# Optimization experiments

Measured on AMD Instinct MI355X. Metric: run time of the kernel, lower is better.

## Reference

```python
import jax, jax.numpy as jnp
import numpy as np

K = 2  # DGL TAGConv default number of hops
N_GRAPHS = 64


def _tag_conv(h, src, dst, W, b, norm):
    # TAGConv: concat [h, A_hat h, A_hat^2 h] @ W + b, A_hat = D^-1/2 A D^-1/2
    n = h.shape[0]
    hops = [h]
    cur = h
    for _ in range(K):
        msg = (cur * norm)[src]                      # gather from src, [E, d]
        agg = jnp.zeros_like(cur).at[dst].add(msg)   # scatter-sum to dst
        cur = agg * norm
        hops.append(cur)
    z = jnp.concatenate(hops, axis=-1)               # [N, (K+1)*d]
    return jax.nn.relu(z @ W + b)


def _norm(dst, n):
    deg = jnp.zeros((n,), jnp.float32).at[dst].add(1.0)
    deg = jnp.clip(deg, 1.0, None)
    return (deg ** -0.5)[:, None]                    # [N, 1]


def setup_inputs() -> dict:
    key = jax.random.key(0)
    ks = jax.random.split(key, 8)
    N, E, IN, HID, C = 100000, 3200000, 128, 256, 10
    h = jax.random.normal(ks[0], (N, IN), jnp.float32)
    src = jax.random.randint(ks[1], (E,), 0, N, jnp.int32)
    dst = jax.random.randint(ks[2], (E,), 0, N, jnp.int32)
    graph_ids = jnp.sort(jax.random.randint(ks[3], (N,), 0, N_GRAPHS, jnp.int32))
    s1 = ((K + 1) * IN) ** -0.5
    s2 = ((K + 1) * HID) ** -0.5
    W1 = jax.random.normal(ks[4], ((K + 1) * IN, HID), jnp.float32) * s1
    b1 = jnp.zeros((HID,), jnp.float32)
    W2 = jax.random.normal(ks[5], ((K + 1) * HID, HID), jnp.float32) * s2
    b2 = jnp.zeros((HID,), jnp.float32)
    Wc = jax.random.normal(ks[6], (HID, C), jnp.float32) * (HID ** -0.5)
    bc = jnp.zeros((C,), jnp.float32)
    return {"h": h, "src": src, "dst": dst, "graph_ids": graph_ids,
            "W1": W1, "b1": b1, "W2": W2, "b2": b2, "Wc": Wc, "bc": bc}


def reference(h, src, dst, graph_ids, W1, b1, W2, b2, Wc, bc):
    n = h.shape[0]
    norm = _norm(dst, n)
    x = _tag_conv(h, src, dst, W1, b1, norm)
    x = _tag_conv(x, src, dst, W2, b2, norm)
    pooled = jax.ops.segment_max(x, graph_ids, num_segments=N_GRAPHS)  # [G, HID]
    return pooled @ Wc + bc                                            # [G, C]
```

## Files before the change

kernel.cpp:

```cpp
#include <hip/hip_runtime.h>
#include <hip/hip_bf16.h>


typedef unsigned short u16;
typedef unsigned int u32;
typedef unsigned char u8;

__device__ inline float u2f(u16 u) { return __uint_as_float(((u32)u) << 16); }
__device__ inline u16 f2u(float f) {
    __hip_bfloat16 b = __float2bfloat16(f);
    return *reinterpret_cast<u16*>(&b);
}


constexpr int NPB = 128, NC = 128, NBMAX = 784;

__global__ __launch_bounds__(256) void countA_kernel(
    const int* __restrict__ dst, int* __restrict__ Hmat, int E, int CS, int NB) {
    __shared__ int hist[NBMAX];
    int tid = threadIdx.x;
    for (int b = tid; b < NB; b += 256) hist[b] = 0;
    __syncthreads();
    int base = blockIdx.x * CS;
    int end = base + CS < E ? base + CS : E;
    for (int i = base + tid; i < end; i += 256) {
        int d = __builtin_nontemporal_load(dst + i);
        atomicAdd(&hist[d >> 7], 1);
    }
    __syncthreads();
    for (int b = tid; b < NB; b += 256) Hmat[b * NC + blockIdx.x] = hist[b];
}

__global__ __launch_bounds__(256) void scatterC_kernel(
    const int* __restrict__ src, const int* __restrict__ dst,
    const int* __restrict__ Omat, uint2* __restrict__ Earr,
    int E, int CS, int NB) {
    __shared__ int cur[NBMAX];
    int tid = threadIdx.x;
    int c = blockIdx.x;
    for (int b = tid; b < NB; b += 256) cur[b] = Omat[b * NC + c];
    __syncthreads();
    int base = c * CS;
    int end = base + CS < E ? base + CS : E;
    for (int i = base + tid; i < end; i += 256) {
        int d = __builtin_nontemporal_load(dst + i);
        int s = __builtin_nontemporal_load(src + i);
        int pos = atomicAdd(&cur[d >> 7], 1);
        uint2 e;
        e.x = (u32)s;
        e.y = (u32)(d & (NPB - 1));
        Earr[pos] = e;
    }
}

__global__ __launch_bounds__(256) void fineD_kernel(
    const uint2* __restrict__ Earr, const int* __restrict__ Omat,
    int* __restrict__ colidx, int* __restrict__ rowptr,
    float* __restrict__ normv, int N, int E, int NB) {
    __shared__ int cnt[NPB];
    __shared__ int scn[NPB];
    __shared__ int cur2[NPB];
    int tid = threadIdx.x;
    int b = blockIdx.x;
    int base = Omat[b * NC];
    int end = Omat[(b + 1) * NC];
    if (tid < NPB) cnt[tid] = 0;
    __syncthreads();
    for (int i = base + tid; i < end; i += 256)
        atomicAdd(&cnt[Earr[i].y], 1);
    __syncthreads();
    if (tid < NPB) scn[tid] = cnt[tid];
    __syncthreads();
    for (int off = 1; off < NPB; off <<= 1) {
        int v = (tid < NPB && tid >= off) ? scn[tid - off] : 0;
        __syncthreads();
        if (tid < NPB) scn[tid] += v;
        __syncthreads();
    }
    int node0 = b * NPB;
    if (tid < NPB) {
        int excl = scn[tid] - cnt[tid];
        cur2[tid] = base + excl;
        int node = node0 + tid;
        if (node < N) {
            rowptr[node] = base + excl;
            int d = cnt[tid];
            float fd = d < 1 ? 1.0f : (float)d;
            normv[node] = rsqrtf(fd);
        }
    }
    if (b == 0 && tid == 0) rowptr[N] = E;
    __syncthreads();
    for (int i = base + tid; i < end; i += 256) {
        uint2 e = Earr[i];
        int pos = atomicAdd(&cur2[e.y], 1);
        colidx[pos] = (int)e.x;
    }
}

__global__ void scan1_kernel(const int* __restrict__ in, int* __restrict__ outp,
                             int* __restrict__ bsum, int n) {
    __shared__ int sd[1024];
    int t = threadIdx.x;
    int i = blockIdx.x * 1024 + t;
    int v = (i < n) ? in[i] : 0;
    sd[t] = v;
    __syncthreads();
    for (int off = 1; off < 1024; off <<= 1) {
        int x = (t >= off) ? sd[t - off] : 0;
        __syncthreads();
        sd[t] += x;
        __syncthreads();
    }
    if (i < n) outp[i] = sd[t] - v;
    if (t == 1023) bsum[blockIdx.x] = sd[t];
}

__global__ void scan2_kernel(int* __restrict__ bsum, int nb) {
    __shared__ int sd[1024];
    int t = threadIdx.x;
    int v = (t < nb) ? bsum[t] : 0;
    sd[t] = v;
    __syncthreads();
    for (int off = 1; off < 1024; off <<= 1) {
        int x = (t >= off) ? sd[t - off] : 0;
        __syncthreads();
        sd[t] += x;
        __syncthreads();
    }
    if (t < nb) bsum[t] = sd[t] - v;
}

__global__ void scan3_kernel(int* __restrict__ outp, const int* __restrict__ bsum,
                             int n, int E) {
    int i = blockIdx.x * blockDim.x + threadIdx.x;
    if (i < n) outp[i] += bsum[i >> 10];
    if (i == 0) outp[n] = E;
}


struct alignas(4) U2 { u16 v[2]; };
struct alignas(8) U4 { u16 v[4]; };
struct alignas(16) U8 { u16 v[8]; };


__global__ __launch_bounds__(256) void castquant_f32_128(
    const float* __restrict__ h, u16* __restrict__ cat, int ldcat,
    const float* __restrict__ normv,
    u8* __restrict__ q, float* __restrict__ m, int N) {
    int row = blockIdx.x * 4 + (threadIdx.x >> 6);
    if (row >= N) return;
    int lane = threadIdx.x & 63;
    float2 f = *(const float2*)(h + (size_t)row * 128 + lane * 2);
    U2 o;
    o.v[0] = f2u(f.x);
    o.v[1] = f2u(f.y);
    *(U2*)(cat + (size_t)row * ldcat + lane * 2) = o;
    float mx = fmaxf(fabsf(f.x), fabsf(f.y));
    #pragma unroll
    for (int off = 32; off > 0; off >>= 1)
        mx = fmaxf(mx, __shfl_xor(mx, off, 64));
    float inv = mx > 0.f ? 127.f / mx : 0.f;
    u32 q0 = (u32)((int)rintf(f.x * inv) + 128);
    u32 q1 = (u32)((int)rintf(f.y * inv) + 128);
    *(unsigned short*)(q + (size_t)row * 128 + lane * 2) =
        (unsigned short)(q0 | (q1 << 8));
    if (lane == 0) m[row] = normv[row] * (mx * (1.f / 127.f));
}


__global__ __launch_bounds__(256) void quant_bf16_256(
    const u16* __restrict__ x, const float* __restrict__ normv,
    u8* __restrict__ q, float* __restrict__ m, int N) {
    int row = blockIdx.x * 4 + (threadIdx.x >> 6);
    if (row >= N) return;
    int lane = threadIdx.x & 63;
    U4 v = *(const U4*)(x + (size_t)row * 256 + lane * 4);
    float f[4];
    #pragma unroll
    for (int i = 0; i < 4; ++i) f[i] = u2f(v.v[i]);
    float mx = fmaxf(fmaxf(fabsf(f[0]), fabsf(f[1])),
                     fmaxf(fabsf(f[2]), fabsf(f[3])));
    #pragma unroll
    for (int off = 32; off > 0; off >>= 1)
        mx = fmaxf(mx, __shfl_xor(mx, off, 64));
    float inv = mx > 0.f ? 127.f / mx : 0.f;
    u32 b0 = (u32)((int)rintf(f[0] * inv) + 128);
    u32 b1 = (u32)((int)rintf(f[1] * inv) + 128);
    u32 b2 = (u32)((int)rintf(f[2] * inv) + 128);
    u32 b3 = (u32)((int)rintf(f[3] * inv) + 128);
    *(u32*)(q + (size_t)row * 256 + lane * 4) =
        b0 | (b1 << 8) | (b2 << 16) | (b3 << 24);
    if (lane == 0) m[row] = normv[row] * (mx * (1.f / 127.f));
}


template <int BPL, int QOUT>
__global__ __launch_bounds__(256, 2) void prop_q8_kernel(
    const u8* __restrict__ qin, const float* __restrict__ m,
    u16* __restrict__ out, int ldout,
    const int* __restrict__ rowptr, const int* __restrict__ colidx,
    const float* __restrict__ normv, int N,
    u8* __restrict__ qout, float* __restrict__ mout) {
    constexpr int D = 32 * BPL;
    constexpr int NW = BPL / 4;
    constexpr int UE = 8;
    int node = blockIdx.x * 4 + (threadIdx.x >> 6);
    if (node >= N) return;
    const int lane = threadIdx.x & 63;
    const int half = lane >> 5;
    const int l32 = lane & 31;
    const u32 laneoff = (u32)l32 * BPL;
    int s = rowptr[node], e = rowptr[node + 1];
    float acc[BPL];
    #pragma unroll
    for (int q = 0; q < BPL; ++q) acc[q] = 0.f;
    float msum = 0.f;
    const int nfull = (e - s) >> 4;
    int p = s;
    if (nfull > 0) {
        int c[UE];
        #pragma unroll
        for (int u = 0; u < UE; ++u) c[u] = colidx[s + 2 * u + half];
        for (int g = 0; g < nfull; ++g) {
            u32 w[UE][NW];
            #pragma unroll
            for (int u = 0; u < UE; ++u) {
                u32 off = (u32)c[u] * D + laneoff;
                if (BPL == 8) {
                    uint2 gg = *(const uint2*)(qin + off);
                    w[u][0] = gg.x; w[u][1] = gg.y;
                } else {
                    w[u][0] = *(const u32*)(qin + off);
                }
            }
            float nm[UE];
            #pragma unroll
            for (int u = 0; u < UE; ++u) nm[u] = m[c[u]];
            if (g + 1 < nfull) {
                int pn = s + (g + 1) * 16;
                #pragma unroll
                for (int u = 0; u < UE; ++u) c[u] = colidx[pn + 2 * u + half];
            }
            #pragma unroll
            for (int u = 0; u < UE; ++u) {
                msum += nm[u];
                #pragma unroll
                for (int t = 0; t < NW; ++t) {
                    u32 ww = w[u][t];
                    acc[4 * t + 0] += nm[u] * (float)(ww & 0xffu);
                    acc[4 * t + 1] += nm[u] * (float)((ww >> 8) & 0xffu);
                    acc[4 * t + 2] += nm[u] * (float)((ww >> 16) & 0xffu);
                    acc[4 * t + 3] += nm[u] * (float)(ww >> 24);
                }
            }
        }
        p = s + nfull * 16;
    }
    if (p < e) {
        const int el = e - 1;
        int c[UE];
        #pragma unroll
        for (int u = 0; u < UE; ++u) {
            int idx = p + 2 * u + half;
            c[u] = colidx[idx < e ? idx : el];
        }
        u32 w[UE][NW];
        #pragma unroll
        for (int u = 0; u < UE; ++u) {
            u32 off = (u32)c[u] * D + laneoff;
            if (BPL == 8) {
                uint2 gg = *(const uint2*)(qin + off);
                w[u][0] = gg.x; w[u][1] = gg.y;
            } else {
                w[u][0] = *(const u32*)(qin + off);
            }
        }
        float nm[UE];
        #pragma unroll
        for (int u = 0; u < UE; ++u) {
            int idx = p + 2 * u + half;
            float mm = m[c[u]];
            nm[u] = idx < e ? mm : 0.f;
        }
        #pragma unroll
        for (int u = 0; u < UE; ++u) {
            msum += nm[u];
            #pragma unroll
            for (int t = 0; t < NW; ++t) {
                u32 ww = w[u][t];
                acc[4 * t + 0] += nm[u] * (float)(ww & 0xffu);
                acc[4 * t + 1] += nm[u] * (float)((ww >> 8) & 0xffu);
                acc[4 * t + 2] += nm[u] * (float)((ww >> 16) & 0xffu);
                acc[4 * t + 3] += nm[u] * (float)(ww >> 24);
            }
        }
    }
    #pragma unroll
    for (int q = 0; q < BPL; ++q) acc[q] += __shfl_xor(acc[q], 32, 64);
    msum += __shfl_xor(msum, 32, 64);
    float nn = normv[node];
    #pragma unroll
    for (int q = 0; q < BPL; ++q) acc[q] = nn * (acc[q] - 128.f * msum);
    if (half == 0) {
        if (BPL == 8) {
            U8 o;
            #pragma unroll
            for (int q = 0; q < 8; ++q) o.v[q] = f2u(acc[q]);
            *(U8*)(out + (size_t)node * ldout + l32 * 8) = o;
        } else {
            U4 o;
            #pragma unroll
            for (int q = 0; q < 4; ++q) o.v[q] = f2u(acc[q]);
            *(U4*)(out + (size_t)node * ldout + l32 * 4) = o;
        }
    }
    if (QOUT) {
        float mx = 0.f;
        #pragma unroll
        for (int q = 0; q < BPL; ++q) mx = fmaxf(mx, fabsf(acc[q]));
        #pragma unroll
        for (int off = 16; off > 0; off >>= 1)
            mx = fmaxf(mx, __shfl_xor(mx, off, 64));
        float inv = mx > 0.f ? 127.f / mx : 0.f;
        if (half == 0) {
            u32 b[BPL > 4 ? 8 : 4];
            #pragma unroll
            for (int q = 0; q < BPL; ++q)
                b[q] = (u32)((int)rintf(acc[q] * inv) + 128);
            if (BPL == 8) {
                uint2 g;
                g.x = b[0] | (b[1] << 8) | (b[2] << 16) | (b[3] << 24);
                g.y = b[4] | (b[5] << 8) | (b[6] << 16) | (b[7] << 24);
                *(uint2*)(qout + (size_t)node * D + l32 * 8) = g;
            } else {
                *(u32*)(qout + (size_t)node * D + l32 * 4) =
                    b[0] | (b[1] << 8) | (b[2] << 16) | (b[3] << 24);
            }
            if (lane == 0) mout[node] = nn * (mx * (1.f / 127.f));
        }
    }
}


typedef __attribute__((ext_vector_type(8))) short bf16x8f;
typedef __attribute__((ext_vector_type(4))) float f32x4;

__device__ inline void async16(const void* g, void* l) {
    __builtin_amdgcn_global_load_lds(
        (__attribute__((address_space(1))) void*)(g),
        (__attribute__((address_space(3))) void*)(l), 16, 0, 0);
}

constexpr int GBM = 128, GBN = 64, GBK = 32;

__device__ inline void stageA_sw(const u16* __restrict__ A, int lda, int row0,
                                 int k0, u16* dst, int tid) {
    #pragma unroll
    for (int i = 0; i < 2; ++i) {
        int c = tid + i * 256;
        int row = c >> 2;
        int seg = (c & 3) ^ ((row >> 1) & 3);
        async16(A + (size_t)(row0 + row) * lda + k0 + seg * 8, dst + c * 8);
    }
}

template <int KK>
__global__ __launch_bounds__(256) void gemm_mfma(
    const u16* __restrict__ A, int lda,
    const u16* __restrict__ Bt,
    const u16* __restrict__ Cadd,
    const float* __restrict__ bias,
    u16* __restrict__ Cout,
    int M, int relu) {
    constexpr int KC = KK / 8;
    __shared__ u16 Ab[2][GBM * GBK];
    __shared__ u16 Bs[GBN * KK];
    const int tid = threadIdx.x;
    const int lane = tid & 63;
    const int wave = tid >> 6;
    const int wm = wave >> 1, wn = wave & 1;
    const int row0 = blockIdx.x * GBM;
    const int col0 = blockIdx.y * GBN;
    const int NOUT = 256;

    {
        const u16* srcB = Bt + (size_t)col0 * KK;
        #pragma unroll
        for (int i = 0; i < GBN * KC / 256; ++i) {
            int cb = tid + i * 256;
            int n = cb / KC;
            int j = (cb % KC) ^ (n & 7);
            async16(srcB + (size_t)n * KK + j * 8, &Bs[cb * 8]);
        }
    }
    stageA_sw(A, lda, row0, 0, Ab[0], tid);
    __syncthreads();

    f32x4 acc[4][2];
    #pragma unroll
    for (int mi = 0; mi < 4; ++mi)
        #pragma unroll
        for (int ni = 0; ni < 2; ++ni) acc[mi][ni] = (f32x4)0.f;

    constexpr int nk = KK / GBK;
    const int mb = lane & 15;
    const int seg = lane >> 4;
    for (int ks = 0; ks < nk; ++ks) {
        int cur = ks & 1;
        if (ks + 1 < nk) stageA_sw(A, lda, row0, (ks + 1) * GBK, Ab[cur ^ 1], tid);
        bf16x8f a[4], b[2];
        #pragma unroll
        for (int mi = 0; mi < 4; ++mi) {
            int r = wm * 64 + mi * 16 + mb;
            int ca = r * 4 + (seg ^ ((r >> 1) & 3));
            a[mi] = *(const bf16x8f*)&Ab[cur][ca * 8];
        }
        #pragma unroll
        for (int ni = 0; ni < 2; ++ni) {
            int n = wn * 32 + ni * 16 + mb;
            int jk = ks * 4 + seg;
            int cb = n * KC + (jk ^ (n & 7));
            b[ni] = *(const bf16x8f*)&Bs[cb * 8];
        }
        #pragma unroll
        for (int mi = 0; mi < 4; ++mi)
            #pragma unroll
            for (int ni = 0; ni < 2; ++ni)
                acc[mi][ni] = __builtin_amdgcn_mfma_f32_16x16x32_bf16(
                    a[mi], b[ni], acc[mi][ni], 0, 0, 0);
        __syncthreads();
    }

    #pragma unroll
    for (int mi = 0; mi < 4; ++mi) {
        #pragma unroll
        for (int r = 0; r < 4; ++r) {
            int row = row0 + wm * 64 + mi * 16 + (lane >> 4) * 4 + r;
            if (row < M) {
                #pragma unroll
                for (int ni = 0; ni < 2; ++ni) {
                    int col = col0 + wn * 32 + ni * 16 + (lane & 15);
                    float v = acc[mi][ni][r];
                    if (Cadd) v += u2f(Cadd[(size_t)row * NOUT + col]);
                    if (bias) v += bias[col];
                    if (relu) v = fmaxf(v, 0.f);
                    Cout[(size_t)row * NOUT + col] = f2u(v);
                }
            }
        }
    }
}

__global__ void transpose_cast(const float* __restrict__ W, u16* __restrict__ Wt,
                               int K, int Nn) {
    int idx = blockIdx.x * blockDim.x + threadIdx.x;
    if (idx < K * Nn) {
        int n = idx / K, k = idx % K;
        Wt[idx] = f2u(W[(size_t)k * Nn + n]);
    }
}


__global__ void pool_kernel(const u16* __restrict__ x, const int* __restrict__ gid,
                            float* __restrict__ pooled, int N, int HID) {
    int t = threadIdx.x;
    int n0 = blockIdx.x * 128;
    int n1 = n0 + 128 < N ? n0 + 128 : N;
    float cur = 0.f;
    int cg = gid[n0];
    for (int n = n0; n < n1; ++n) {
        int g = gid[n];
        if (g != cg) {
            atomicMax((int*)&pooled[(size_t)cg * HID + t], __float_as_int(cur));
            cg = g;
            cur = 0.f;
        }
        float v = u2f(x[(size_t)n * HID + t]);
        cur = cur > v ? cur : v;
    }
    atomicMax((int*)&pooled[(size_t)cg * HID + t], __float_as_int(cur));
}

__global__ void head_kernel(const float* __restrict__ pooled, const float* __restrict__ Wc,
                            const float* __restrict__ bc, float* __restrict__ out,
                            int HID, int C) {
    __shared__ float row[256];
    int g = blockIdx.x;
    int t = threadIdx.x;
    if (t < HID) row[t] = pooled[(size_t)g * HID + t];
    __syncthreads();
    if (t < C) {
        float s = bc[t];
        for (int k = 0; k < HID; ++k) s += row[k] * Wc[(size_t)k * C + t];
        out[(size_t)g * C + t] = s;
    }
}


extern "C" void kernel_launch(void* const* d_in, const int* in_sizes, int n_in,
                              void* d_out, int out_size, void* d_ws, size_t ws_size,
                              hipStream_t stream) {
    const float* h  = (const float*)d_in[0];
    const int* src  = (const int*)d_in[1];
    const int* dst  = (const int*)d_in[2];
    const int* gid  = (const int*)d_in[3];
    const float* W1 = (const float*)d_in[4];
    const float* b1 = (const float*)d_in[5];
    const float* W2 = (const float*)d_in[6];
    const float* b2 = (const float*)d_in[7];
    const float* Wc = (const float*)d_in[8];
    const float* bc = (const float*)d_in[9];
    float* out = (float*)d_out;

    const int N   = in_sizes[3];
    const int E   = in_sizes[1];
    const int IN  = in_sizes[0] / N;
    const int HID = in_sizes[5];
    const int C   = in_sizes[9];
    const int G   = out_size / C;
    const int CAT = 3 * IN;
    const int Mpad = (N + 127) & ~127;
    const int NB = (N + NPB - 1) / NPB;
    const int CS = (E + NC - 1) / NC;

    char* wp = (char*)d_ws;
    auto alloc = [&](size_t bytes) {
        char* p = wp;
        wp += (bytes + 255) & ~(size_t)255;
        return p;
    };
    float* pooled = (float*)alloc((size_t)G * HID * sizeof(float));
    float* normv  = (float*)alloc((size_t)N * sizeof(float));
    float* mv     = (float*)alloc((size_t)N * sizeof(float));
    float* mv2    = (float*)alloc((size_t)N * sizeof(float));
    int* rowptr   = (int*)alloc((size_t)(N + 1) * sizeof(int));
    int* bsum     = (int*)alloc(1024 * sizeof(int));
    int* Omat     = (int*)alloc((size_t)(NB * NC + 1) * sizeof(int));
    int* Hmat     = (int*)alloc((size_t)(NB * NC) * sizeof(int));
    int* colidx   = (int*)alloc((size_t)E * sizeof(int));
    u16* Wt1      = (u16*)alloc((size_t)CAT * HID * sizeof(u16));
    u16* Wt2      = (u16*)alloc((size_t)3 * HID * HID * sizeof(u16));
    u16* CAT1     = (u16*)alloc((size_t)Mpad * CAT * sizeof(u16));
    u16* X1       = (u16*)alloc((size_t)Mpad * HID * sizeof(u16));
    u16* B2       = (u16*)alloc((size_t)Mpad * HID * sizeof(u16));
    u16* B1       = CAT1;
    uint2* Earr   = (uint2*)CAT1;
    u8* Q8L2      = (u8*)(CAT1 + (size_t)Mpad * HID);
    u8* Q8A       = (u8*)B2;
    u8* Q8B       = (u8*)B2 + (size_t)Mpad * 128;

    const int n2 = NB * NC;
    countA_kernel<<<NC, 256, 0, stream>>>(dst, Hmat, E, CS, NB);
    scan1_kernel<<<(n2 + 1023) / 1024, 1024, 0, stream>>>(Hmat, Omat, bsum, n2);
    scan2_kernel<<<1, 1024, 0, stream>>>(bsum, (n2 + 1023) / 1024);
    scan3_kernel<<<(n2 + 255) / 256, 256, 0, stream>>>(Omat, bsum, n2, E);
    scatterC_kernel<<<NC, 256, 0, stream>>>(src, dst, Omat, Earr, E, CS, NB);
    fineD_kernel<<<NB, 256, 0, stream>>>(Earr, Omat, colidx, rowptr, normv, N, E, NB);

    transpose_cast<<<(CAT * HID + 255) / 256, 256, 0, stream>>>(W1, Wt1, CAT, HID);
    for (int s2 = 0; s2 < 3; ++s2)
        transpose_cast<<<(HID * HID + 255) / 256, 256, 0, stream>>>(
            W2 + (size_t)s2 * HID * HID, Wt2 + (size_t)s2 * HID * HID, HID, HID);

    int pb = (N + 3) / 4;
    castquant_f32_128<<<pb, 256, 0, stream>>>(h, CAT1, CAT, normv, Q8A, mv, N);
    prop_q8_kernel<4, 1><<<pb, 256, 0, stream>>>(Q8A, mv, CAT1 + IN, CAT,
                                                 rowptr, colidx, normv, N, Q8B, mv2);
    prop_q8_kernel<4, 0><<<pb, 256, 0, stream>>>(Q8B, mv2, CAT1 + 2 * IN, CAT,
                                                 rowptr, colidx, normv, N,
                                                 nullptr, nullptr);
    dim3 ggrid(Mpad / GBM, HID / GBN);
    gemm_mfma<384><<<ggrid, 256, 0, stream>>>(CAT1, CAT, Wt1, nullptr, b1, X1, N, 1);

    gemm_mfma<256><<<ggrid, 256, 0, stream>>>(X1, HID, Wt2 + (size_t)2 * HID * HID,
                                              nullptr, nullptr, B1, N, 0);
    quant_bf16_256<<<pb, 256, 0, stream>>>(B1, normv, Q8L2, mv, N);
    prop_q8_kernel<8, 0><<<pb, 256, 0, stream>>>(Q8L2, mv, B2, HID,
                                                 rowptr, colidx, normv, N,
                                                 nullptr, nullptr);
    gemm_mfma<256><<<ggrid, 256, 0, stream>>>(X1, HID, Wt2 + (size_t)HID * HID,
                                              B2, nullptr, B1, N, 0);
    quant_bf16_256<<<pb, 256, 0, stream>>>(B1, normv, Q8L2, mv, N);
    prop_q8_kernel<8, 0><<<pb, 256, 0, stream>>>(Q8L2, mv, B2, HID,
                                                 rowptr, colidx, normv, N,
                                                 nullptr, nullptr);
    gemm_mfma<256><<<ggrid, 256, 0, stream>>>(X1, HID, Wt2, B2, b2, B1, N, 1);

    hipMemsetAsync(pooled, 0, (size_t)G * HID * sizeof(float), stream);
    pool_kernel<<<(N + 127) / 128, HID, 0, stream>>>(B1, gid, pooled, N, HID);
    head_kernel<<<G, HID, 0, stream>>>(pooled, Wc, bc, out, HID, C);
}
```

Before: 1.045 ms.

## Fuse int8 quantization into GEMM epilogue with per-32-column scales, remap grid

Removes the separate quant_bf16_256 pass by quantizing GEMM outputs to int8 directly in the epilogue. Scales are now computed per 32-column group, so each row has 8 scale factors, and the propagation kernel reads the scale for its lane's column group. The GEMM is also launched as a 1D grid with an XCD-aware block remapping. This avoids writing and re-reading the bf16 intermediate, at the cost of extra shuffles, an LDS staging pass in the epilogue, and 8x more scale reads in propagation.

```diff
diff --git a/kernel.cpp b/kernel.cpp
--- a/kernel.cpp
+++ b/kernel.cpp
@@ -169,33 +169,7 @@
 }
 
 
-__global__ __launch_bounds__(256) void quant_bf16_256(
-    const u16* __restrict__ x, const float* __restrict__ normv,
-    u8* __restrict__ q, float* __restrict__ m, int N) {
-    int row = blockIdx.x * 4 + (threadIdx.x >> 6);
-    if (row >= N) return;
-    int lane = threadIdx.x & 63;
-    U4 v = *(const U4*)(x + (size_t)row * 256 + lane * 4);
-    float f[4];
-    #pragma unroll
-    for (int i = 0; i < 4; ++i) f[i] = u2f(v.v[i]);
-    float mx = fmaxf(fmaxf(fabsf(f[0]), fabsf(f[1])),
-                     fmaxf(fabsf(f[2]), fabsf(f[3])));
-    #pragma unroll
-    for (int off = 32; off > 0; off >>= 1)
-        mx = fmaxf(mx, __shfl_xor(mx, off, 64));
-    float inv = mx > 0.f ? 127.f / mx : 0.f;
-    u32 b0 = (u32)((int)rintf(f[0] * inv) + 128);
-    u32 b1 = (u32)((int)rintf(f[1] * inv) + 128);
-    u32 b2 = (u32)((int)rintf(f[2] * inv) + 128);
-    u32 b3 = (u32)((int)rintf(f[3] * inv) + 128);
-    *(u32*)(q + (size_t)row * 256 + lane * 4) =
-        b0 | (b1 << 8) | (b2 << 16) | (b3 << 24);
-    if (lane == 0) m[row] = normv[row] * (mx * (1.f / 127.f));
-}
-
-
-template <int BPL, int QOUT>
+template <int BPL, int QOUT, int SGRP>
 __global__ __launch_bounds__(256, 2) void prop_q8_kernel(
     const u8* __restrict__ qin, const float* __restrict__ m,
     u16* __restrict__ out, int ldout,
@@ -211,6 +185,7 @@
     const int half = lane >> 5;
     const int l32 = lane & 31;
     const u32 laneoff = (u32)l32 * BPL;
+    const u32 soff = (SGRP == 8) ? (u32)(l32 >> 2) : 0u;
     int s = rowptr[node], e = rowptr[node + 1];
     float acc[BPL];
     #pragma unroll
@@ -236,7 +211,7 @@
             }
             float nm[UE];
             #pragma unroll
-            for (int u = 0; u < UE; ++u) nm[u] = m[c[u]];
+            for (int u = 0; u < UE; ++u) nm[u] = m[(u32)c[u] * SGRP + soff];
             if (g + 1 < nfull) {
                 int pn = s + (g + 1) * 16;
                 #pragma unroll
@@ -280,7 +255,7 @@
         #pragma unroll
         for (int u = 0; u < UE; ++u) {
             int idx = p + 2 * u + half;
-            float mm = m[c[u]];
+            float mm = m[(u32)c[u] * SGRP + soff];
             nm[u] = idx < e ? mm : 0.f;
         }
         #pragma unroll
@@ -365,13 +340,16 @@
     }
 }
 
-template <int KK>
+template <int KK, int QMODE>
 __global__ __launch_bounds__(256) void gemm_mfma(
     const u16* __restrict__ A, int lda,
     const u16* __restrict__ Bt,
     const u16* __restrict__ Cadd,
     const float* __restrict__ bias,
     u16* __restrict__ Cout,
+    u8* __restrict__ Qout,
+    float* __restrict__ Mout,
+    const float* __restrict__ normv,
     int M, int relu) {
     constexpr int KC = KK / 8;
     __shared__ u16 Ab[2][GBM * GBK];
@@ -380,8 +358,11 @@
     const int lane = tid & 63;
     const int wave = tid >> 6;
     const int wm = wave >> 1, wn = wave & 1;
-    const int row0 = blockIdx.x * GBM;
-    const int col0 = blockIdx.y * GBN;
+    int nwg = gridDim.x;
+    int q8c = nwg >> 3;
+    int nb = (blockIdx.x & 7) * q8c + (blockIdx.x >> 3);
+    const int row0 = (nb >> 2) * GBM;
+    const int col0 = (nb & 3) * GBN;
     const int NOUT = 256;
 
     {
@@ -432,22 +413,76 @@
         __syncthreads();
     }
 
-    #pragma unroll
-    for (int mi = 0; mi < 4; ++mi) {
-        #pragma unroll
-        for (int r = 0; r < 4; ++r) {
-            int row = row0 + wm * 64 + mi * 16 + (lane >> 4) * 4 + r;
-            if (row < M) {
+    if (QMODE == 0) {
+        #pragma unroll
+        for (int mi = 0; mi < 4; ++mi) {
+            #pragma unroll
+            for (int r = 0; r < 4; ++r) {
+                int row = row0 + wm * 64 + mi * 16 + (lane >> 4) * 4 + r;
+                if (row < M) {
+                    #pragma unroll
+                    for (int ni = 0; ni < 2; ++ni) {
+                        int col = col0 + wn * 32 + ni * 16 + (lane & 15);
+                        float v = acc[mi][ni][r];
+                        if (Cadd) v += u2f(Cadd[(size_t)row * NOUT + col]);
+                        if (bias) v += bias[col];
+                        if (relu) v = fmaxf(v, 0.f);
+                        Cout[(size_t)row * NOUT + col] = f2u(v);
+                    }
+                }
+            }
+        }
+    } else {
+        u8* q8s = (u8*)Ab;
+        float v[4][2][4];
+        #pragma unroll
+        for (int mi = 0; mi < 4; ++mi) {
+            #pragma unroll
+            for (int r = 0; r < 4; ++r) {
+                int row = row0 + wm * 64 + mi * 16 + (lane >> 4) * 4 + r;
+                bool ok = row < M;
                 #pragma unroll
                 for (int ni = 0; ni < 2; ++ni) {
                     int col = col0 + wn * 32 + ni * 16 + (lane & 15);
-                    float v = acc[mi][ni][r];
-                    if (Cadd) v += u2f(Cadd[(size_t)row * NOUT + col]);
-                    if (bias) v += bias[col];
-                    if (relu) v = fmaxf(v, 0.f);
-                    Cout[(size_t)row * NOUT + col] = f2u(v);
+                    float x = acc[mi][ni][r];
+                    if (Cadd && ok) x += u2f(Cadd[(size_t)row * NOUT + col]);
+                    v[mi][ni][r] = x;
                 }
             }
+        }
+        #pragma unroll
+        for (int mi = 0; mi < 4; ++mi) {
+            #pragma unroll
+            for (int r = 0; r < 4; ++r) {
+                float mx = fmaxf(fabsf(v[mi][0][r]), fabsf(v[mi][1][r]));
+                #pragma unroll
+                for (int off = 1; off < 16; off <<= 1)
+                    mx = fmaxf(mx, __shfl_xor(mx, off, 64));
+                float inv = mx > 0.f ? 127.f / mx : 0.f;
+                int rl = wm * 64 + mi * 16 + (lane >> 4) * 4 + r;
+                #pragma unroll
+                for (int ni = 0; ni < 2; ++ni) {
+                    int b = (int)rintf(v[mi][ni][r] * inv) + 128;
+                    q8s[rl * 64 + wn * 32 + ni * 16 + (lane & 15)] = (u8)b;
+                }
+                if ((lane & 15) == 0) {
+                    int row = row0 + rl;
+                    if (row < M)
+                        Mout[(size_t)row * 8 + (col0 >> 5) + wn] =
+                            normv[row] * (mx * (1.f / 127.f));
+                }
+            }
+        }
+        __syncthreads();
+        #pragma unroll
+        for (int i = 0; i < 2; ++i) {
+            int cidx = tid * 2 + i;
+            int rl = cidx >> 2;
+            int co = (cidx & 3) * 16;
+            int row = row0 + rl;
+            if (row < M)
+                *(uint4*)(Qout + (size_t)row * 256 + col0 + co) =
+                    *(const uint4*)(q8s + rl * 64 + co);
         }
     }
 }
@@ -534,6 +569,7 @@
     float* normv  = (float*)alloc((size_t)N * sizeof(float));
     float* mv     = (float*)alloc((size_t)N * sizeof(float));
     float* mv2    = (float*)alloc((size_t)N * sizeof(float));
+    float* mv8    = (float*)alloc((size_t)Mpad * 8 * sizeof(float));
     int* rowptr   = (int*)alloc((size_t)(N + 1) * sizeof(int));
     int* bsum     = (int*)alloc(1024 * sizeof(int));
     int* Omat     = (int*)alloc((size_t)(NB * NC + 1) * sizeof(int));
@@ -565,27 +601,29 @@
 
     int pb = (N + 3) / 4;
     castquant_f32_128<<<pb, 256, 0, stream>>>(h, CAT1, CAT, normv, Q8A, mv, N);
-    prop_q8_kernel<4, 1><<<pb, 256, 0, stream>>>(Q8A, mv, CAT1 + IN, CAT,
-                                                 rowptr, colidx, normv, N, Q8B, mv2);
-    prop_q8_kernel<4, 0><<<pb, 256, 0, stream>>>(Q8B, mv2, CAT1 + 2 * IN, CAT,
-                                                 rowptr, colidx, normv, N,
-                                                 nullptr, nullptr);
-    dim3 ggrid(Mpad / GBM, HID / GBN);
-    gemm_mfma<384><<<ggrid, 256, 0, stream>>>(CAT1, CAT, Wt1, nullptr, b1, X1, N, 1);
-
-    gemm_mfma<256><<<ggrid, 256, 0, stream>>>(X1, HID, Wt2 + (size_t)2 * HID * HID,
-                                              nullptr, nullptr, B1, N, 0);
-    quant_bf16_256<<<pb, 256, 0, stream>>>(B1, normv, Q8L2, mv, N);
-    prop_q8_kernel<8, 0><<<pb, 256, 0, stream>>>(Q8L2, mv, B2, HID,
-                                                 rowptr, colidx, normv, N,
-                                                 nullptr, nullptr);
-    gemm_mfma<256><<<ggrid, 256, 0, stream>>>(X1, HID, Wt2 + (size_t)HID * HID,
-                                              B2, nullptr, B1, N, 0);
-    quant_bf16_256<<<pb, 256, 0, stream>>>(B1, normv, Q8L2, mv, N);
-    prop_q8_kernel<8, 0><<<pb, 256, 0, stream>>>(Q8L2, mv, B2, HID,
-                                                 rowptr, colidx, normv, N,
-                                                 nullptr, nullptr);
-    gemm_mfma<256><<<ggrid, 256, 0, stream>>>(X1, HID, Wt2, B2, b2, B1, N, 1);
+    prop_q8_kernel<4, 1, 1><<<pb, 256, 0, stream>>>(Q8A, mv, CAT1 + IN, CAT,
+                                                    rowptr, colidx, normv, N, Q8B, mv2);
+    prop_q8_kernel<4, 0, 1><<<pb, 256, 0, stream>>>(Q8B, mv2, CAT1 + 2 * IN, CAT,
+                                                    rowptr, colidx, normv, N,
+                                                    nullptr, nullptr);
+    int nwg = (Mpad / GBM) * (HID / GBN);
+    gemm_mfma<384, 0><<<nwg, 256, 0, stream>>>(CAT1, CAT, Wt1, nullptr, b1, X1,
+                                               nullptr, nullptr, nullptr, N, 1);
+
+    gemm_mfma<256, 1><<<nwg, 256, 0, stream>>>(X1, HID, Wt2 + (size_t)2 * HID * HID,
+                                               nullptr, nullptr, nullptr,
+                                               Q8L2, mv8, normv, N, 0);
+    prop_q8_kernel<8, 0, 8><<<pb, 256, 0, stream>>>(Q8L2, mv8, B2, HID,
+                                                    rowptr, colidx, normv, N,
+                                                    nullptr, nullptr);
+    gemm_mfma<256, 1><<<nwg, 256, 0, stream>>>(X1, HID, Wt2 + (size_t)HID * HID,
+                                               B2, nullptr, nullptr,
+                                               Q8L2, mv8, normv, N, 0);
+    prop_q8_kernel<8, 0, 8><<<pb, 256, 0, stream>>>(Q8L2, mv8, B2, HID,
+                                                    rowptr, colidx, normv, N,
+                                                    nullptr, nullptr);
+    gemm_mfma<256, 0><<<nwg, 256, 0, stream>>>(X1, HID, Wt2, B2, b2, B1,
+                                               nullptr, nullptr, nullptr, N, 1);
 
     hipMemsetAsync(pooled, 0, (size_t)G * HID * sizeof(float), stream);
     pool_kernel<<<(N + 127) / 128, HID, 0, stream>>>(B1, gid, pooled, N, HID);
```

Result: slower. 1.077 ms (+3.1%).

## Widen GEMM tile to 128x128 with streamed B panels and XCD-aware block mapping

Applied to the files above, without the earlier changes.

The MFMA GEMM tile grows from 128x64 to 128x128, so each wave computes 4x4 MFMA fragments and each A panel is reused across twice as many output columns. Instead of loading the whole B slab into LDS up front, B is now double-buffered in 32-wide K panels alongside A. A 1D grid is remapped so consecutive tiles land on the same XCD, which should improve L2 locality, with the two column tiles of a row block adjacent. The trade-off is more accumulator registers and possibly lower occupancy, and it halves the number of workgroups.

```diff
diff --git a/kernel.cpp b/kernel.cpp
--- a/kernel.cpp
+++ b/kernel.cpp
@@ -352,16 +352,16 @@
         (__attribute__((address_space(3))) void*)(l), 16, 0, 0);
 }
 
-constexpr int GBM = 128, GBN = 64, GBK = 32;
-
-__device__ inline void stageA_sw(const u16* __restrict__ A, int lda, int row0,
-                                 int k0, u16* dst, int tid) {
+constexpr int GBM = 128, GBN = 128, GBK = 32;
+
+__device__ inline void stage_panel(const u16* __restrict__ P, int ldp, int row0,
+                                   int k0, u16* dst, int tid) {
     #pragma unroll
     for (int i = 0; i < 2; ++i) {
         int c = tid + i * 256;
         int row = c >> 2;
         int seg = (c & 3) ^ ((row >> 1) & 3);
-        async16(A + (size_t)(row0 + row) * lda + k0 + seg * 8, dst + c * 8);
+        async16(P + (size_t)(row0 + row) * ldp + k0 + seg * 8, dst + c * 8);
     }
 }
 
@@ -373,43 +373,40 @@
     const float* __restrict__ bias,
     u16* __restrict__ Cout,
     int M, int relu) {
-    constexpr int KC = KK / 8;
     __shared__ u16 Ab[2][GBM * GBK];
-    __shared__ u16 Bs[GBN * KK];
+    __shared__ u16 Bb[2][GBN * GBK];
     const int tid = threadIdx.x;
     const int lane = tid & 63;
     const int wave = tid >> 6;
     const int wm = wave >> 1, wn = wave & 1;
-    const int row0 = blockIdx.x * GBM;
-    const int col0 = blockIdx.y * GBN;
+    int nwg = gridDim.x;
+    int qq = nwg >> 3, rr = nwg & 7;
+    int xcd = blockIdx.x & 7, wi = blockIdx.x >> 3;
+    int nb = (xcd < rr ? xcd * (qq + 1) : rr * (qq + 1) + (xcd - rr) * qq) + wi;
+    const int row0 = (nb >> 1) * GBM;
+    const int col0 = (nb & 1) * GBN;
     const int NOUT = 256;
 
-    {
-        const u16* srcB = Bt + (size_t)col0 * KK;
-        #pragma unroll
-        for (int i = 0; i < GBN * KC / 256; ++i) {
-            int cb = tid + i * 256;
-            int n = cb / KC;
-            int j = (cb % KC) ^ (n & 7);
-            async16(srcB + (size_t)n * KK + j * 8, &Bs[cb * 8]);
-        }
-    }
-    stageA_sw(A, lda, row0, 0, Ab[0], tid);
-    __syncthreads();
-
-    f32x4 acc[4][2];
+    stage_panel(A, lda, row0, 0, Ab[0], tid);
+    stage_panel(Bt, KK, col0, 0, Bb[0], tid);
+    __syncthreads();
+
+    f32x4 acc[4][4];
     #pragma unroll
     for (int mi = 0; mi < 4; ++mi)
         #pragma unroll
-        for (int ni = 0; ni < 2; ++ni) acc[mi][ni] = (f32x4)0.f;
+        for (int ni = 0; ni < 4; ++ni) acc[mi][ni] = (f32x4)0.f;
 
     constexpr int nk = KK / GBK;
     const int mb = lane & 15;
     const int seg = lane >> 4;
     for (int ks = 0; ks < nk; ++ks) {
         int cur = ks & 1;
-        if (ks + 1 < nk) stageA_sw(A, lda, row0, (ks + 1) * GBK, Ab[cur ^ 1], tid);
-        bf16x8f a[4], b[2];
+        if (ks + 1 < nk) {
+            stage_panel(A, lda, row0, (ks + 1) * GBK, Ab[cur ^ 1], tid);
+            stage_panel(Bt, KK, col0, (ks + 1) * GBK, Bb[cur ^ 1], tid);
+        }
+        bf16x8f a[4], b[4];
         #pragma unroll
         for (int mi = 0; mi < 4; ++mi) {
             int r = wm * 64 + mi * 16 + mb;
@@ -417,16 +414,15 @@
             a[mi] = *(const bf16x8f*)&Ab[cur][ca * 8];
         }
         #pragma unroll
-        for (int ni = 0; ni < 2; ++ni) {
-            int n = wn * 32 + ni * 16 + mb;
-            int jk = ks * 4 + seg;
-            int cb = n * KC + (jk ^ (n & 7));
-            b[ni] = *(const bf16x8f*)&Bs[cb * 8];
+        for (int ni = 0; ni < 4; ++ni) {
+            int n = wn * 64 + ni * 16 + mb;
+            int cb = n * 4 + (seg ^ ((n >> 1) & 3));
+            b[ni] = *(const bf16x8f*)&Bb[cur][cb * 8];
         }
         #pragma unroll
         for (int mi = 0; mi < 4; ++mi)
             #pragma unroll
-            for (int ni = 0; ni < 2; ++ni)
+            for (int ni = 0; ni < 4; ++ni)
                 acc[mi][ni] = __builtin_amdgcn_mfma_f32_16x16x32_bf16(
                     a[mi], b[ni], acc[mi][ni], 0, 0, 0);
         __syncthreads();
@@ -439,8 +435,8 @@
             int row = row0 + wm * 64 + mi * 16 + (lane >> 4) * 4 + r;
             if (row < M) {
                 #pragma unroll
-                for (int ni = 0; ni < 2; ++ni) {
-                    int col = col0 + wn * 32 + ni * 16 + (lane & 15);
+                for (int ni = 0; ni < 4; ++ni) {
+                    int col = col0 + wn * 64 + ni * 16 + (lane & 15);
                     float v = acc[mi][ni][r];
                     if (Cadd) v += u2f(Cadd[(size_t)row * NOUT + col]);
                     if (bias) v += bias[col];
@@ -570,22 +566,22 @@
     prop_q8_kernel<4, 0><<<pb, 256, 0, stream>>>(Q8B, mv2, CAT1 + 2 * IN, CAT,
                                                  rowptr, colidx, normv, N,
                                                  nullptr, nullptr);
-    dim3 ggrid(Mpad / GBM, HID / GBN);
-    gemm_mfma<384><<<ggrid, 256, 0, stream>>>(CAT1, CAT, Wt1, nullptr, b1, X1, N, 1);
-
-    gemm_mfma<256><<<ggrid, 256, 0, stream>>>(X1, HID, Wt2 + (size_t)2 * HID * HID,
-                                              nullptr, nullptr, B1, N, 0);
+    int nwg = (Mpad / GBM) * (HID / GBN);
+    gemm_mfma<384><<<nwg, 256, 0, stream>>>(CAT1, CAT, Wt1, nullptr, b1, X1, N, 1);
+
+    gemm_mfma<256><<<nwg, 256, 0, stream>>>(X1, HID, Wt2 + (size_t)2 * HID * HID,
+                                            nullptr, nullptr, B1, N, 0);
     quant_bf16_256<<<pb, 256, 0, stream>>>(B1, normv, Q8L2, mv, N);
     prop_q8_kernel<8, 0><<<pb, 256, 0, stream>>>(Q8L2, mv, B2, HID,
                                                  rowptr, colidx, normv, N,
                                                  nullptr, nullptr);
-    gemm_mfma<256><<<ggrid, 256, 0, stream>>>(X1, HID, Wt2 + (size_t)HID * HID,
-                                              B2, nullptr, B1, N, 0);
+    gemm_mfma<256><<<nwg, 256, 0, stream>>>(X1, HID, Wt2 + (size_t)HID * HID,
+                                            B2, nullptr, B1, N, 0);
     quant_bf16_256<<<pb, 256, 0, stream>>>(B1, normv, Q8L2, mv, N);
     prop_q8_kernel<8, 0><<<pb, 256, 0, stream>>>(Q8L2, mv, B2, HID,
                                                  rowptr, colidx, normv, N,
                                                  nullptr, nullptr);
-    gemm_mfma<256><<<ggrid, 256, 0, stream>>>(X1, HID, Wt2, B2, b2, B1, N, 1);
+    gemm_mfma<256><<<nwg, 256, 0, stream>>>(X1, HID, Wt2, B2, b2, B1, N, 1);
 
     hipMemsetAsync(pooled, 0, (size_t)G * HID * sizeof(float), stream);
     pool_kernel<<<(N + 127) / 128, HID, 0, stream>>>(B1, gid, pooled, N, HID);
```

Result: no change. 1.050 ms (+0.4%).
